# Performance work log

Hardware: AMD Instinct MI355X
Metric: run time of the kernel (lower is better)

## Reference

```python
import jax, jax.numpy as jnp
import numpy as np

B, S, EMB, H = 2, 2048, 1024, 16
D = EMB // H  # per-head dim = 64
SCALE = 1.0 / np.sqrt(D).astype(np.float32)


def setup_inputs() -> dict:
    key = jax.random.key(0)
    ks = jax.random.split(key, 11)
    lim = 1.0 / np.sqrt(EMB).astype(np.float32)  # torch Linear default init range
    def lin(kw, kb):
        W = jax.random.uniform(kw, (EMB, EMB), jnp.float32, -lim, lim)
        b = jax.random.uniform(kb, (EMB,), jnp.float32, -lim, lim)
        return W, b
    Wq, bq = lin(ks[0], ks[1])
    Wk, bk = lin(ks[2], ks[3])
    Wv, bv = lin(ks[4], ks[5])
    Wo, bo = lin(ks[6], ks[7])
    xq = jax.random.normal(ks[8], (B, S, EMB), jnp.float32)
    xk = jax.random.normal(ks[9], (B, S, EMB), jnp.float32)
    xv = jax.random.normal(ks[10], (B, S, EMB), jnp.float32)
    mask = jnp.tril(jnp.ones((S, S), dtype=jnp.int32))  # causal mask; 0 -> blocked
    return {"xq": xq, "xk": xk, "xv": xv, "mask": mask,
            "Wq": Wq, "bq": bq, "Wk": Wk, "bk": bk,
            "Wv": Wv, "bv": bv, "Wo": Wo, "bo": bo}


def reference(xq, xk, xv, mask, Wq, bq, Wk, bk, Wv, bv, Wo, bo):
    # Projections (torch Linear: x @ W.T + b), then split heads: [B,S,E] -> [B,H,S,D]
    def split_heads(x):
        return x.reshape(B, S, H, D).transpose(0, 2, 1, 3)
    Q = split_heads(xq @ Wq.T + bq)
    K = split_heads(xk @ Wk.T + bk)
    V = split_heads(xv @ Wv.T + bv)
    scores = jnp.einsum("bhqd,bhkd->bhqk", Q, K) * SCALE  # [B,H,S,S]
    scores = jnp.where(mask[None, None, :, :] == 0, jnp.float32(-1e9), scores)
    attn = jax.nn.softmax(scores, axis=-1)  # softmax over key axis (dim=2 per-head in torch)
    res = jnp.einsum("bhqk,bhkd->bhqd", attn, V)
    res = res.transpose(0, 2, 1, 3).reshape(B, S, EMB)  # merge heads back (same slicing layout)
    return res @ Wo.T + bo
```

## Files before the change

### kernel.cpp

```cpp
#include <hip/hip_runtime.h>
#include <hip/hip_bf16.h>

#define BB   2
#define SS   2048
#define EMBD 1024
#define NH   16
#define HD   64
#define QSCALE 0.18033688011112042f
#define NEG_BIG (-1e30f)

typedef __bf16 bf16;
typedef float  floatx4 __attribute__((ext_vector_type(4)));
typedef __bf16 bf16x4  __attribute__((ext_vector_type(4)));
typedef __bf16 bf16x8  __attribute__((ext_vector_type(8)));

typedef const __attribute__((address_space(1))) void* gas_ptr;
typedef __attribute__((address_space(3))) void*       las_ptr;

__device__ __forceinline__ void gl_lds16(const void* g, void* l) {
    __builtin_amdgcn_global_load_lds((gas_ptr)g, (las_ptr)l, 16, 0, 0);
}

__device__ __forceinline__ bf16x8 cvt8(const float* p) {
    bf16x8 o;
#pragma unroll
    for (int j = 0; j < 8; j++) o[j] = (bf16)p[j];
    return o;
}

__global__ __launch_bounds__(256) void cvt_all(
    const float* __restrict__ xq, const float* __restrict__ xk,
    const float* __restrict__ xv, const float* __restrict__ Wq,
    const float* __restrict__ Wk, const float* __restrict__ Wv,
    const float* __restrict__ Wo, bf16* __restrict__ xqo,
    bf16* __restrict__ xko, bf16* __restrict__ xvo, bf16* __restrict__ Wqo,
    bf16* __restrict__ Wko, bf16* __restrict__ Wvo, bf16* __restrict__ Woo) {
    const int y = blockIdx.y;
    const float* src;
    bf16* dst;
    size_t n;
    const size_t NX = (size_t)BB * SS * EMBD;
    const size_t NW = (size_t)EMBD * EMBD;
    switch (y) {
        case 0: src = xq; dst = xqo; n = NX; break;
        case 1: src = xk; dst = xko; n = NX; break;
        case 2: src = xv; dst = xvo; n = NX; break;
        case 3: src = Wq; dst = Wqo; n = NW; break;
        case 4: src = Wk; dst = Wko; n = NW; break;
        case 5: src = Wv; dst = Wvo; n = NW; break;
        default: src = Wo; dst = Woo; n = NW; break;
    }
    const size_t stride = (size_t)gridDim.x * blockDim.x * 4;
    for (size_t i = ((size_t)blockIdx.x * blockDim.x + threadIdx.x) * 4;
         i < n; i += stride) {
        floatx4 v = *(const floatx4*)(src + i);
        bf16x4 o = {(bf16)v[0], (bf16)v[1], (bf16)v[2], (bf16)v[3]};
        *(bf16x4*)(dst + i) = o;
    }
}

extern __shared__ __align__(16) char smem[];

template <int MODE, int FM>
__device__ __forceinline__ void gemm_body(const bf16* __restrict__ A,
                                          const bf16* __restrict__ W,
                                          const float* __restrict__ bias,
                                          void* __restrict__ Ov,
                                          int mBase, int nBase, float oscale) {
    constexpr int BM = 32 * FM;
    constexpr int ABYTES = BM * 64 * 2;
    bf16* As = (bf16*)smem;
    bf16* Bs = (bf16*)(smem + ABYTES);

    const int t = threadIdx.x;
    const int l = t & 63, w = t >> 6;
    const int lm = l & 15, lq = l >> 4;
    const int K = 1024;
    const int wm = (w >> 1) * (16 * FM), wn = (w & 1) * 64;

    const floatx4 zero = {0.f, 0.f, 0.f, 0.f};
    floatx4 acc[FM][4];
#pragma unroll
    for (int i = 0; i < FM; i++)
#pragma unroll
        for (int j = 0; j < 4; j++) acc[i][j] = zero;

    for (int kb = 0; kb < K; kb += 64) {
        __syncthreads();
#pragma unroll
        for (int ia = 0; ia < FM; ia++) {
            int half = ia / (FM / 2 > 0 ? FM / 2 : 1);
            int rem  = (ia % (FM / 2 > 0 ? FM / 2 : 1)) * 256 + t;
            int row  = rem >> 2;
            int col  = half * 32 + (rem & 3) * 8;
            gl_lds16(A + (size_t)(mBase + row) * K + kb + col,
                     (char*)As + (ia * 256 + w * 64) * 16);
        }
#pragma unroll
        for (int i = 0; i < 4; i++) {
            int half = i >> 1;
            int rem  = (i & 1) * 256 + t;
            int row  = rem >> 2;
            int col  = half * 32 + (rem & 3) * 8;
            gl_lds16(W + (size_t)(nBase + row) * K + kb + col,
                     (char*)Bs + (i * 256 + w * 64) * 16);
        }
        __syncthreads();

#pragma unroll
        for (int half = 0; half < 2; half++) {
            const bf16* Ah = As + half * BM * 32;
            const bf16* Bh = Bs + half * 128 * 32;
            bf16x8 af[FM], bfv[4];
#pragma unroll
            for (int f = 0; f < FM; f++)
                af[f] = *(const bf16x8*)&Ah[(wm + f * 16 + lm) * 32 + lq * 8];
#pragma unroll
            for (int f = 0; f < 4; f++)
                bfv[f] = *(const bf16x8*)&Bh[(wn + f * 16 + lm) * 32 + lq * 8];
            if (MODE == 2) {
#pragma unroll
                for (int i = 0; i < 4; i++)
#pragma unroll
                    for (int j = 0; j < FM; j++)
                        acc[j][i] = __builtin_amdgcn_mfma_f32_16x16x32_bf16(
                            bfv[i], af[j], acc[j][i], 0, 0, 0);
            } else {
#pragma unroll
                for (int fm = 0; fm < FM; fm++)
#pragma unroll
                    for (int fn = 0; fn < 4; fn++)
                        acc[fm][fn] =
                            __builtin_amdgcn_mfma_f32_16x16x32_bf16(
                                af[fm], bfv[fn], acc[fm][fn], 0, 0, 0);
            }
        }
    }

    __syncthreads();
    float* rp = (float*)smem + w * (16 * 68);

    if (MODE != 2) {
        float bvv[4];
#pragma unroll
        for (int fn = 0; fn < 4; fn++)
            bvv[fn] = bias[nBase + wn + fn * 16 + lm];
#pragma unroll
        for (int fm = 0; fm < FM; fm++) {
#pragma unroll
            for (int fn = 0; fn < 4; fn++)
#pragma unroll
                for (int r = 0; r < 4; r++)
                    rp[(lq * 4 + r) * 68 + fn * 16 + lm] =
                        (acc[fm][fn][r] + bvv[fn]) * oscale;
            if (MODE == 0) {
                int row2 = l >> 3, col8 = l & 7;
                int h = (nBase + wn) >> 6;
#pragma unroll
                for (int p = 0; p < 2; p++) {
                    int row = p * 8 + row2;
                    int m = mBase + wm + fm * 16 + row;
                    int b = m >> 11, s = m & 2047;
                    bf16x8 o = cvt8(&rp[row * 68 + col8 * 8]);
                    *(bf16x8*)((bf16*)Ov +
                               (((size_t)(b * NH + h)) * SS + s) * HD +
                               col8 * 8) = o;
                }
            } else {
                int c4 = l & 15;
#pragma unroll
                for (int p = 0; p < 4; p++) {
                    int row = p * 4 + (l >> 4);
                    int m = mBase + wm + fm * 16 + row;
                    floatx4 o = *(const floatx4*)&rp[row * 68 + c4 * 4];
                    *(floatx4*)((float*)Ov + (size_t)m * EMBD + nBase + wn +
                                c4 * 4) = o;
                }
            }
        }
    } else {
        const int b = (mBase + wm) >> 11;
        const int sbase = (mBase + wm) & 2047;
#pragma unroll
        for (int i = 0; i < 4; i++) {
            float bv[4];
#pragma unroll
            for (int r = 0; r < 4; r++)
                bv[r] = bias[nBase + wn + i * 16 + lq * 4 + r];
#pragma unroll
            for (int j = 0; j < FM; j++)
#pragma unroll
                for (int r = 0; r < 4; r++)
                    rp[(lq * 4 + r) * 68 + j * 16 + lm] =
                        acc[j][i][r] + bv[r];
            int row2 = l >> 3, col8 = l & 7;
#pragma unroll
            for (int p = 0; p < 2; p++) {
                int row = p * 8 + row2;
                int n = nBase + wn + i * 16 + row;
                int h = n >> 6, d = n & 63;
                bf16x8 o = cvt8(&rp[row * 68 + col8 * 8]);
                *(bf16x8*)((bf16*)Ov +
                           ((size_t)(b * NH + h) * HD + d) * SS + sbase +
                           col8 * 8) = o;
            }
        }
    }
}

__global__ __launch_bounds__(256, 4) void gemm_qkv(
    const bf16* __restrict__ xq, const bf16* __restrict__ xk,
    const bf16* __restrict__ xv, const bf16* __restrict__ Wq,
    const bf16* __restrict__ Wk, const bf16* __restrict__ Wv,
    const float* __restrict__ bq, const float* __restrict__ bk,
    const float* __restrict__ bv, bf16* __restrict__ Qo,
    bf16* __restrict__ Ko, bf16* __restrict__ Vo) {
    const int z = blockIdx.z;
    const int mB = blockIdx.x * 128, nB = blockIdx.y * 128;
    if (z == 0)
        gemm_body<0, 4>(xq, Wq, bq, Qo, mB, nB, QSCALE);
    else if (z == 1)
        gemm_body<0, 4>(xk, Wk, bk, Ko, mB, nB, 1.0f);
    else
        gemm_body<2, 4>(xv, Wv, bv, Vo, mB, nB, 1.0f);
}

__global__ __launch_bounds__(256, 4) void gemm_out(
    const bf16* __restrict__ A, const bf16* __restrict__ W,
    const float* __restrict__ bias, float* __restrict__ O) {
    gemm_body<1, 2>(A, W, bias, O, blockIdx.x * 64, blockIdx.y * 128, 1.0f);
}

__global__ __launch_bounds__(256, 3) void attn_fwd(
    const bf16* __restrict__ Qg, const bf16* __restrict__ Kg,
    const bf16* __restrict__ Vtg, bf16* __restrict__ Oatt) {
    __shared__ __align__(16) bf16 Ksb[2 * 64 * 64];
    __shared__ __align__(16) bf16 VTb[2 * 64 * 64];
    __shared__ __align__(16) bf16 Ps[4][16 * 64];

    const int t = threadIdx.x;
    const int l = t & 63, w = t >> 6;
    const int lm = l & 15, lq = l >> 4;
    const int m7 = lm & 7;
    const int x = blockIdx.x;
    const int i5 = x >> 5;
    const int gq = i5 >> 3, jq = i5 & 7;
    const int qt = (gq == 0) ? jq
                 : (gq == 1) ? 15 - jq
                 : (gq == 2) ? 16 + jq
                             : 31 - jq;
    const int bh = (((x >> 3) & 3) << 3) | (x & 7);
    const size_t kbase = (size_t)bh * SS * HD;
    const size_t vbase = (size_t)bh * HD * SS;
    const int b = bh >> 4, h = bh & 15;
    const floatx4 zero = {0.f, 0.f, 0.f, 0.f};

    const int trow = t >> 3, tsl = t & 7;
    const int cswz = ((tsl ^ (trow & 7)) << 3);
    const bf16* kgp = Kg + kbase + (size_t)trow * HD + cswz;
    const bf16* vgp = Vtg + vbase + (size_t)trow * SS + cswz;
    bf16* ksd = Ksb + t * 8;
    bf16* vtd = VTb + t * 8;

    bf16x8 qa0, qa1;
    {
        const bf16* qp =
            Qg + kbase + (size_t)(qt * 64 + w * 16 + lm) * HD + lq * 8;
        qa0 = *(const bf16x8*)qp;
        qa1 = *(const bf16x8*)(qp + 32);
    }

    float m_i = NEG_BIG, l_i = 0.f;
    floatx4 od[4];
#pragma unroll
    for (int dt = 0; dt < 4; dt++) od[dt] = zero;

    const int qglob = qt * 64 + w * 16 + lm;

    gl_lds16(kgp, ksd);
    gl_lds16(kgp + 2048, ksd + 2048);
    gl_lds16(vgp, vtd);
    gl_lds16(vgp + 32 * SS, vtd + 2048);
    __syncthreads();

    for (int kt = 0; kt <= qt; ++kt) {
        const int cur = kt & 1;
        const bf16* Kc = Ksb + cur * 4096;
        const bf16* Vc = VTb + cur * 4096;
        if (kt < qt) {
            const bf16* kp = kgp + (size_t)(kt + 1) * 4096;
            const bf16* vp = vgp + (size_t)(kt + 1) * 64;
            bf16* kn = ksd + (cur ^ 1) * 4096;
            bf16* vn = vtd + (cur ^ 1) * 4096;
            gl_lds16(kp, kn);
            gl_lds16(kp + 2048, kn + 2048);
            gl_lds16(vp, vn);
            gl_lds16(vp + 32 * SS, vn + 2048);
        }

        floatx4 sc[4];
#pragma unroll
        for (int j0 = 0; j0 < 4; j0++) {
            int rowK = j0 * 16 + lm;
            bf16x8 k0 = *(const bf16x8*)&Kc[rowK * 64 + ((lq ^ m7) << 3)];
            bf16x8 k1 =
                *(const bf16x8*)&Kc[rowK * 64 + (((4 + lq) ^ m7) << 3)];
            floatx4 z = zero;
            z = __builtin_amdgcn_mfma_f32_16x16x32_bf16(k0, qa0, z, 0, 0, 0);
            z = __builtin_amdgcn_mfma_f32_16x16x32_bf16(k1, qa1, z, 0, 0, 0);
            sc[j0] = z;
        }
        if (kt == qt) {
#pragma unroll
            for (int j0 = 0; j0 < 4; j0++)
#pragma unroll
                for (int r = 0; r < 4; r++) {
                    int key = kt * 64 + j0 * 16 + lq * 4 + r;
                    if (key > qglob) sc[j0][r] = NEG_BIG;
                }
        }
        float m4[4];
#pragma unroll
        for (int a = 0; a < 4; a++)
            m4[a] = fmaxf(fmaxf(sc[a][0], sc[a][1]),
                          fmaxf(sc[a][2], sc[a][3]));
        float mt = fmaxf(fmaxf(m4[0], m4[1]), fmaxf(m4[2], m4[3]));
        mt = fmaxf(mt, __shfl_xor(mt, 16));
        mt = fmaxf(mt, __shfl_xor(mt, 32));
        float mnew = fmaxf(m_i, mt);
        float alpha = __builtin_amdgcn_exp2f(m_i - mnew);
        m_i = mnew;
        float psa0 = 0.f, psa1 = 0.f, psa2 = 0.f, psa3 = 0.f;
#pragma unroll
        for (int j0 = 0; j0 < 4; j0++) {
            float p0 = __builtin_amdgcn_exp2f(sc[j0][0] - mnew);
            float p1 = __builtin_amdgcn_exp2f(sc[j0][1] - mnew);
            float p2 = __builtin_amdgcn_exp2f(sc[j0][2] - mnew);
            float p3 = __builtin_amdgcn_exp2f(sc[j0][3] - mnew);
            sc[j0][0] = p0; sc[j0][1] = p1;
            sc[j0][2] = p2; sc[j0][3] = p3;
            psa0 += p0; psa1 += p1; psa2 += p2; psa3 += p3;
        }
        float ps = (psa0 + psa1) + (psa2 + psa3);
        ps += __shfl_xor(ps, 16);
        ps += __shfl_xor(ps, 32);
        l_i = l_i * alpha + ps;
        float a0 = __shfl(alpha, lq * 4 + 0);
        float a1 = __shfl(alpha, lq * 4 + 1);
        float a2 = __shfl(alpha, lq * 4 + 2);
        float a3 = __shfl(alpha, lq * 4 + 3);
#pragma unroll
        for (int dt = 0; dt < 4; dt++) {
            od[dt][0] *= a0;
            od[dt][1] *= a1;
            od[dt][2] *= a2;
            od[dt][3] *= a3;
        }
#pragma unroll
        for (int j0l = 0; j0l < 4; j0l++) {
            floatx4 s4 = sc[j0l];
            bf16x4 pk = {(bf16)s4[0], (bf16)s4[1], (bf16)s4[2], (bf16)s4[3]};
            *(bf16x4*)&Ps[w][lm * 64 + ((j0l * 16 + lq * 4) ^ (m7 * 8))] = pk;
        }
        bf16x8 pa0 = *(const bf16x8*)&Ps[w][lm * 64 + ((lq * 8) ^ (m7 * 8))];
        bf16x8 pa1 =
            *(const bf16x8*)&Ps[w][lm * 64 + ((32 + lq * 8) ^ (m7 * 8))];
#pragma unroll
        for (int dt = 0; dt < 4; dt++) {
            int rowD = dt * 16 + lm;
            bf16x8 v0 = *(const bf16x8*)&Vc[rowD * 64 + ((lq ^ m7) << 3)];
            od[dt] = __builtin_amdgcn_mfma_f32_16x16x32_bf16(pa0, v0, od[dt],
                                                             0, 0, 0);
            bf16x8 v1 =
                *(const bf16x8*)&Vc[rowD * 64 + (((4 + lq) ^ m7) << 3)];
            od[dt] = __builtin_amdgcn_mfma_f32_16x16x32_bf16(pa1, v1, od[dt],
                                                             0, 0, 0);
        }
        __syncthreads();
    }

    float linv = 1.0f / l_i;
    float lr0 = __shfl(linv, lq * 4 + 0);
    float lr1 = __shfl(linv, lq * 4 + 1);
    float lr2 = __shfl(linv, lq * 4 + 2);
    float lr3 = __shfl(linv, lq * 4 + 3);
    float lr[4] = {lr0, lr1, lr2, lr3};
#pragma unroll
    for (int dt = 0; dt < 4; dt++) {
#pragma unroll
        for (int r = 0; r < 4; r++) {
            int s = qt * 64 + w * 16 + lq * 4 + r;
            float v = od[dt][r] * lr[r];
            Oatt[((size_t)(b * SS + s)) * EMBD + h * HD + dt * 16 + lm] =
                (bf16)v;
        }
    }
}

extern "C" void kernel_launch(void* const* d_in, const int* in_sizes, int n_in,
                              void* d_out, int out_size, void* d_ws,
                              size_t ws_size, hipStream_t stream) {
    const float* xq = (const float*)d_in[0];
    const float* xk = (const float*)d_in[1];
    const float* xv = (const float*)d_in[2];
    const float* Wq = (const float*)d_in[4];
    const float* bq = (const float*)d_in[5];
    const float* Wk = (const float*)d_in[6];
    const float* bk = (const float*)d_in[7];
    const float* Wv = (const float*)d_in[8];
    const float* bv = (const float*)d_in[9];
    const float* Wo = (const float*)d_in[10];
    const float* bo = (const float*)d_in[11];
    float* out = (float*)d_out;

    const size_t NX = (size_t)BB * SS * EMBD;
    const size_t NW = (size_t)EMBD * EMBD;
    bf16* Qw  = (bf16*)d_ws;
    bf16* Kw  = Qw + NX;
    bf16* Vw  = Kw + NX;
    bf16* Aw  = Vw + NX;
    bf16* xqb = Aw + NX;
    bf16* xkb = xqb + NX;
    bf16* xvb = xkb + NX;
    bf16* Wqb = xvb + NX;
    bf16* Wkb = Wqb + NW;
    bf16* Wvb = Wkb + NW;
    bf16* Wob = Wvb + NW;

    cvt_all<<<dim3(1024, 7), 256, 0, stream>>>(xq, xk, xv, Wq, Wk, Wv, Wo,
                                               xqb, xkb, xvb, Wqb, Wkb, Wvb,
                                               Wob);
    gemm_qkv<<<dim3(32, 8, 3), 256, 32768, stream>>>(
        xqb, xkb, xvb, Wqb, Wkb, Wvb, bq, bk, bv, Qw, Kw, Vw);
    attn_fwd<<<dim3(1024), 256, 0, stream>>>(Qw, Kw, Vw, Aw);
    gemm_out<<<dim3(64, 8), 256, 24576, stream>>>(Aw, Wob, bo, out);
}
```

Measured before the change: 224.1 us.

## Split long causal query tiles across two blocks and merge partials

The attention kernel now splits the KV range of the 16 longest query tiles into two halves run by separate blocks, writes fp32 partial outputs with row max and sum to reused workspace, and merges them in a new small kernel. This aims to balance the causal workload and shorten the critical path of the longest blocks. It also defers the online-softmax rescale unless the max grows past a threshold, and raises wave priority around MFMA sections. The cost is an extra kernel launch and fp32 partial traffic. Deferred rescaling risks exp overflow only if scores jump by a large margin.

```diff
diff --git a/kernel.cpp b/kernel.cpp
--- a/kernel.cpp
+++ b/kernel.cpp
@@ -8,6 +8,7 @@
 #define HD   64
 #define QSCALE 0.18033688011112042f
 #define NEG_BIG (-1e30f)
+#define DEFER_THR 6.0f
 
 typedef __bf16 bf16;
 typedef float  floatx4 __attribute__((ext_vector_type(4)));
@@ -233,7 +234,9 @@
 
 __global__ __launch_bounds__(256, 3) void attn_fwd(
     const bf16* __restrict__ Qg, const bf16* __restrict__ Kg,
-    const bf16* __restrict__ Vtg, bf16* __restrict__ Oatt) {
+    const bf16* __restrict__ Vtg, bf16* __restrict__ Oatt,
+    float* __restrict__ pod, float* __restrict__ pmw,
+    float* __restrict__ plw) {
     __shared__ __align__(16) bf16 Ksb[2 * 64 * 64];
     __shared__ __align__(16) bf16 VTb[2 * 64 * 64];
     __shared__ __align__(16) bf16 Ps[4][16 * 64];
@@ -244,11 +247,21 @@
     const int m7 = lm & 7;
     const int x = blockIdx.x;
     const int i5 = x >> 5;
-    const int gq = i5 >> 3, jq = i5 & 7;
-    const int qt = (gq == 0) ? jq
-                 : (gq == 1) ? 15 - jq
-                 : (gq == 2) ? 16 + jq
-                             : 31 - jq;
+    int qt, cbeg, cend, split, half;
+    if (i5 < 32) {
+        qt = 31 - (i5 >> 1);
+        half = i5 & 1;
+        int nch = qt + 1, chalf = (nch + 1) >> 1;
+        cbeg = half ? chalf : 0;
+        cend = half ? nch : chalf;
+        split = 1;
+    } else {
+        qt = 47 - i5;
+        half = 0;
+        cbeg = 0;
+        cend = qt + 1;
+        split = 0;
+    }
     const int bh = (((x >> 3) & 3) << 3) | (x & 7);
     const size_t kbase = (size_t)bh * SS * HD;
     const size_t vbase = (size_t)bh * HD * SS;
@@ -277,17 +290,17 @@
 
     const int qglob = qt * 64 + w * 16 + lm;
 
-    gl_lds16(kgp, ksd);
-    gl_lds16(kgp + 2048, ksd + 2048);
-    gl_lds16(vgp, vtd);
-    gl_lds16(vgp + 32 * SS, vtd + 2048);
+    gl_lds16(kgp + (size_t)cbeg * 4096, ksd);
+    gl_lds16(kgp + (size_t)cbeg * 4096 + 2048, ksd + 2048);
+    gl_lds16(vgp + (size_t)cbeg * 64, vtd);
+    gl_lds16(vgp + (size_t)cbeg * 64 + 32 * SS, vtd + 2048);
     __syncthreads();
 
-    for (int kt = 0; kt <= qt; ++kt) {
-        const int cur = kt & 1;
+    for (int kt = cbeg; kt < cend; ++kt) {
+        const int cur = (kt - cbeg) & 1;
         const bf16* Kc = Ksb + cur * 4096;
         const bf16* Vc = VTb + cur * 4096;
-        if (kt < qt) {
+        if (kt + 1 < cend) {
             const bf16* kp = kgp + (size_t)(kt + 1) * 4096;
             const bf16* vp = vgp + (size_t)(kt + 1) * 64;
             bf16* kn = ksd + (cur ^ 1) * 4096;
@@ -299,6 +312,7 @@
         }
 
         floatx4 sc[4];
+        __builtin_amdgcn_s_setprio(1);
 #pragma unroll
         for (int j0 = 0; j0 < 4; j0++) {
             int rowK = j0 * 16 + lm;
@@ -310,6 +324,7 @@
             z = __builtin_amdgcn_mfma_f32_16x16x32_bf16(k1, qa1, z, 0, 0, 0);
             sc[j0] = z;
         }
+        __builtin_amdgcn_s_setprio(0);
         if (kt == qt) {
 #pragma unroll
             for (int j0 = 0; j0 < 4; j0++)
@@ -327,16 +342,30 @@
         float mt = fmaxf(fmaxf(m4[0], m4[1]), fmaxf(m4[2], m4[3]));
         mt = fmaxf(mt, __shfl_xor(mt, 16));
         mt = fmaxf(mt, __shfl_xor(mt, 32));
-        float mnew = fmaxf(m_i, mt);
-        float alpha = __builtin_amdgcn_exp2f(m_i - mnew);
-        m_i = mnew;
+        if (__any(mt > m_i + DEFER_THR)) {
+            float mnew = fmaxf(m_i, mt);
+            float alpha = __builtin_amdgcn_exp2f(m_i - mnew);
+            m_i = mnew;
+            l_i *= alpha;
+            float a0 = __shfl(alpha, lq * 4 + 0);
+            float a1 = __shfl(alpha, lq * 4 + 1);
+            float a2 = __shfl(alpha, lq * 4 + 2);
+            float a3 = __shfl(alpha, lq * 4 + 3);
+#pragma unroll
+            for (int dt = 0; dt < 4; dt++) {
+                od[dt][0] *= a0;
+                od[dt][1] *= a1;
+                od[dt][2] *= a2;
+                od[dt][3] *= a3;
+            }
+        }
         float psa0 = 0.f, psa1 = 0.f, psa2 = 0.f, psa3 = 0.f;
 #pragma unroll
         for (int j0 = 0; j0 < 4; j0++) {
-            float p0 = __builtin_amdgcn_exp2f(sc[j0][0] - mnew);
-            float p1 = __builtin_amdgcn_exp2f(sc[j0][1] - mnew);
-            float p2 = __builtin_amdgcn_exp2f(sc[j0][2] - mnew);
-            float p3 = __builtin_amdgcn_exp2f(sc[j0][3] - mnew);
+            float p0 = __builtin_amdgcn_exp2f(sc[j0][0] - m_i);
+            float p1 = __builtin_amdgcn_exp2f(sc[j0][1] - m_i);
+            float p2 = __builtin_amdgcn_exp2f(sc[j0][2] - m_i);
+            float p3 = __builtin_amdgcn_exp2f(sc[j0][3] - m_i);
             sc[j0][0] = p0; sc[j0][1] = p1;
             sc[j0][2] = p2; sc[j0][3] = p3;
             psa0 += p0; psa1 += p1; psa2 += p2; psa3 += p3;
@@ -344,18 +373,7 @@
         float ps = (psa0 + psa1) + (psa2 + psa3);
         ps += __shfl_xor(ps, 16);
         ps += __shfl_xor(ps, 32);
-        l_i = l_i * alpha + ps;
-        float a0 = __shfl(alpha, lq * 4 + 0);
-        float a1 = __shfl(alpha, lq * 4 + 1);
-        float a2 = __shfl(alpha, lq * 4 + 2);
-        float a3 = __shfl(alpha, lq * 4 + 3);
-#pragma unroll
-        for (int dt = 0; dt < 4; dt++) {
-            od[dt][0] *= a0;
-            od[dt][1] *= a1;
-            od[dt][2] *= a2;
-            od[dt][3] *= a3;
-        }
+        l_i += ps;
 #pragma unroll
         for (int j0l = 0; j0l < 4; j0l++) {
             floatx4 s4 = sc[j0l];
@@ -365,6 +383,7 @@
         bf16x8 pa0 = *(const bf16x8*)&Ps[w][lm * 64 + ((lq * 8) ^ (m7 * 8))];
         bf16x8 pa1 =
             *(const bf16x8*)&Ps[w][lm * 64 + ((32 + lq * 8) ^ (m7 * 8))];
+        __builtin_amdgcn_s_setprio(1);
 #pragma unroll
         for (int dt = 0; dt < 4; dt++) {
             int rowD = dt * 16 + lm;
@@ -376,25 +395,81 @@
             od[dt] = __builtin_amdgcn_mfma_f32_16x16x32_bf16(pa1, v1, od[dt],
                                                              0, 0, 0);
         }
+        __builtin_amdgcn_s_setprio(0);
         __syncthreads();
     }
 
-    float linv = 1.0f / l_i;
-    float lr0 = __shfl(linv, lq * 4 + 0);
-    float lr1 = __shfl(linv, lq * 4 + 1);
-    float lr2 = __shfl(linv, lq * 4 + 2);
-    float lr3 = __shfl(linv, lq * 4 + 3);
-    float lr[4] = {lr0, lr1, lr2, lr3};
-#pragma unroll
-    for (int dt = 0; dt < 4; dt++) {
-#pragma unroll
-        for (int r = 0; r < 4; r++) {
-            int s = qt * 64 + w * 16 + lq * 4 + r;
-            float v = od[dt][r] * lr[r];
-            Oatt[((size_t)(b * SS + s)) * EMBD + h * HD + dt * 16 + lm] =
-                (bf16)v;
-        }
-    }
+    if (split) {
+        const int pp = (((qt - 16) << 5) | bh) * 2 + half;
+        float* po = pod + (size_t)pp * 4096;
+#pragma unroll
+        for (int dt = 0; dt < 4; dt++)
+#pragma unroll
+            for (int r = 0; r < 4; r++)
+                po[(w * 16 + lq * 4 + r) * 64 + dt * 16 + lm] = od[dt][r];
+        if (lq == 0) {
+            pmw[pp * 64 + w * 16 + lm] = m_i;
+            plw[pp * 64 + w * 16 + lm] = l_i;
+        }
+    } else {
+        float linv = 1.0f / l_i;
+        float lr0 = __shfl(linv, lq * 4 + 0);
+        float lr1 = __shfl(linv, lq * 4 + 1);
+        float lr2 = __shfl(linv, lq * 4 + 2);
+        float lr3 = __shfl(linv, lq * 4 + 3);
+        float lr[4] = {lr0, lr1, lr2, lr3};
+#pragma unroll
+        for (int dt = 0; dt < 4; dt++) {
+#pragma unroll
+            for (int r = 0; r < 4; r++) {
+                int s = qt * 64 + w * 16 + lq * 4 + r;
+                float v = od[dt][r] * lr[r];
+                Oatt[((size_t)(b * SS + s)) * EMBD + h * HD + dt * 16 + lm] =
+                    (bf16)v;
+            }
+        }
+    }
+}
+
+__global__ __launch_bounds__(256) void attn_merge(
+    const float* __restrict__ pod, const float* __restrict__ pmw,
+    const float* __restrict__ plw, bf16* __restrict__ Oatt) {
+    const int p = blockIdx.x;
+    const int qt = 16 + (p >> 5), bh = p & 31;
+    const int b = bh >> 4, h = bh & 15;
+    const int t = threadIdx.x;
+    const int q = t >> 2, d0 = (t & 3) * 16;
+    const int pp0 = p * 2, pp1 = pp0 + 1;
+    const float m0 = pmw[pp0 * 64 + q], m1 = pmw[pp1 * 64 + q];
+    const float l0 = plw[pp0 * 64 + q], l1 = plw[pp1 * 64 + q];
+    const float mm = fmaxf(m0, m1);
+    const float a0 = __builtin_amdgcn_exp2f(m0 - mm);
+    const float a1 = __builtin_amdgcn_exp2f(m1 - mm);
+    const float inv = 1.0f / (l0 * a0 + l1 * a1);
+    const float w0 = a0 * inv, w1 = a1 * inv;
+    const float* o0 = pod + ((size_t)pp0 * 64 + q) * 64 + d0;
+    const float* o1 = pod + ((size_t)pp1 * 64 + q) * 64 + d0;
+    bf16* dst =
+        Oatt + ((size_t)(b * SS + qt * 64 + q)) * EMBD + h * HD + d0;
+    bf16x8 oa, ob;
+#pragma unroll
+    for (int i = 0; i < 2; i++) {
+        floatx4 v0 = *(const floatx4*)(o0 + i * 4);
+        floatx4 v1 = *(const floatx4*)(o1 + i * 4);
+#pragma unroll
+        for (int r = 0; r < 4; r++)
+            oa[i * 4 + r] = (bf16)(v0[r] * w0 + v1[r] * w1);
+    }
+#pragma unroll
+    for (int i = 0; i < 2; i++) {
+        floatx4 v0 = *(const floatx4*)(o0 + 8 + i * 4);
+        floatx4 v1 = *(const floatx4*)(o1 + 8 + i * 4);
+#pragma unroll
+        for (int r = 0; r < 4; r++)
+            ob[i * 4 + r] = (bf16)(v0[r] * w0 + v1[r] * w1);
+    }
+    *(bf16x8*)dst = oa;
+    *(bf16x8*)(dst + 8) = ob;
 }
 
 extern "C" void kernel_launch(void* const* d_in, const int* in_sizes, int n_in,
@@ -426,12 +501,16 @@
     bf16* Wkb = Wqb + NW;
     bf16* Wvb = Wkb + NW;
     bf16* Wob = Wvb + NW;
+    float* pod = (float*)xqb;
+    float* pmw = (float*)xvb;
+    float* plw = pmw + 1024 * 64;
 
     cvt_all<<<dim3(1024, 7), 256, 0, stream>>>(xq, xk, xv, Wq, Wk, Wv, Wo,
                                                xqb, xkb, xvb, Wqb, Wkb, Wvb,
                                                Wob);
     gemm_qkv<<<dim3(32, 8, 3), 256, 32768, stream>>>(
         xqb, xkb, xvb, Wqb, Wkb, Wvb, bq, bk, bv, Qw, Kw, Vw);
-    attn_fwd<<<dim3(1024), 256, 0, stream>>>(Qw, Kw, Vw, Aw);
+    attn_fwd<<<dim3(1536), 256, 0, stream>>>(Qw, Kw, Vw, Aw, pod, pmw, plw);
+    attn_merge<<<dim3(512), 256, 0, stream>>>(pod, pmw, plw, Aw);
     gemm_out<<<dim3(64, 8), 256, 24576, stream>>>(Aw, Wob, bo, out);
 }
```

Measured after the change: 227.9 us. Within noise of the previous version (+1.7%).

## Process two query fragments per wave with 2-wave blocks and deferred rescale

Applied to the files above, without the earlier changes.

The attention kernel now runs with 128 threads (2 waves), each wave handling 32 query rows as two 16-row fragments. This reuses each K/V fragment read from LDS across two MFMAs, so LDS traffic per unit of compute drops. It also adds a lazy online-softmax rescale that skips the accumulator rescale unless the running max grows past a threshold, and uses s_setprio around the MFMA sections. In exchange each wave needs more registers and there are fewer waves per block to hide latency.

```diff
diff --git a/kernel.cpp b/kernel.cpp
--- a/kernel.cpp
+++ b/kernel.cpp
@@ -8,6 +8,7 @@
 #define HD   64
 #define QSCALE 0.18033688011112042f
 #define NEG_BIG (-1e30f)
+#define DEFER_THR 6.0f
 
 typedef __bf16 bf16;
 typedef float  floatx4 __attribute__((ext_vector_type(4)));
@@ -231,12 +232,12 @@
     gemm_body<1, 2>(A, W, bias, O, blockIdx.x * 64, blockIdx.y * 128, 1.0f);
 }
 
-__global__ __launch_bounds__(256, 3) void attn_fwd(
+__global__ __launch_bounds__(128, 2) void attn_fwd(
     const bf16* __restrict__ Qg, const bf16* __restrict__ Kg,
     const bf16* __restrict__ Vtg, bf16* __restrict__ Oatt) {
     __shared__ __align__(16) bf16 Ksb[2 * 64 * 64];
     __shared__ __align__(16) bf16 VTb[2 * 64 * 64];
-    __shared__ __align__(16) bf16 Ps[4][16 * 64];
+    __shared__ __align__(16) bf16 Ps[2][32 * 64];
 
     const int t = threadIdx.x;
     const int l = t & 63, w = t >> 6;
@@ -259,28 +260,29 @@
     const int cswz = ((tsl ^ (trow & 7)) << 3);
     const bf16* kgp = Kg + kbase + (size_t)trow * HD + cswz;
     const bf16* vgp = Vtg + vbase + (size_t)trow * SS + cswz;
-    bf16* ksd = Ksb + t * 8;
-    bf16* vtd = VTb + t * 8;
-
-    bf16x8 qa0, qa1;
-    {
-        const bf16* qp =
-            Qg + kbase + (size_t)(qt * 64 + w * 16 + lm) * HD + lq * 8;
-        qa0 = *(const bf16x8*)qp;
-        qa1 = *(const bf16x8*)(qp + 32);
-    }
-
-    float m_i = NEG_BIG, l_i = 0.f;
-    floatx4 od[4];
-#pragma unroll
-    for (int dt = 0; dt < 4; dt++) od[dt] = zero;
-
-    const int qglob = qt * 64 + w * 16 + lm;
-
-    gl_lds16(kgp, ksd);
-    gl_lds16(kgp + 2048, ksd + 2048);
-    gl_lds16(vgp, vtd);
-    gl_lds16(vgp + 32 * SS, vtd + 2048);
+
+    bf16x8 qa[2][2];
+#pragma unroll
+    for (int f = 0; f < 2; f++) {
+        const bf16* qp = Qg + kbase +
+                         (size_t)(qt * 64 + w * 32 + f * 16 + lm) * HD +
+                         lq * 8;
+        qa[f][0] = *(const bf16x8*)qp;
+        qa[f][1] = *(const bf16x8*)(qp + 32);
+    }
+
+    float m_i[2] = {NEG_BIG, NEG_BIG}, l_i[2] = {0.f, 0.f};
+    floatx4 od[2][4];
+#pragma unroll
+    for (int f = 0; f < 2; f++)
+#pragma unroll
+        for (int dt = 0; dt < 4; dt++) od[f][dt] = zero;
+
+#pragma unroll
+    for (int i = 0; i < 4; i++) {
+        gl_lds16(kgp + (size_t)i * 1024, Ksb + i * 1024 + t * 8);
+        gl_lds16(vgp + (size_t)i * 16 * SS, VTb + i * 1024 + t * 8);
+    }
     __syncthreads();
 
     for (int kt = 0; kt <= qt; ++kt) {
@@ -290,109 +292,157 @@
         if (kt < qt) {
             const bf16* kp = kgp + (size_t)(kt + 1) * 4096;
             const bf16* vp = vgp + (size_t)(kt + 1) * 64;
-            bf16* kn = ksd + (cur ^ 1) * 4096;
-            bf16* vn = vtd + (cur ^ 1) * 4096;
-            gl_lds16(kp, kn);
-            gl_lds16(kp + 2048, kn + 2048);
-            gl_lds16(vp, vn);
-            gl_lds16(vp + 32 * SS, vn + 2048);
-        }
-
-        floatx4 sc[4];
+            bf16* kn = Ksb + (cur ^ 1) * 4096 + t * 8;
+            bf16* vn = VTb + (cur ^ 1) * 4096 + t * 8;
+#pragma unroll
+            for (int i = 0; i < 4; i++) {
+                gl_lds16(kp + (size_t)i * 1024, kn + i * 1024);
+                gl_lds16(vp + (size_t)i * 16 * SS, vn + i * 1024);
+            }
+        }
+
+        floatx4 sc[2][4];
+        __builtin_amdgcn_s_setprio(1);
 #pragma unroll
         for (int j0 = 0; j0 < 4; j0++) {
             int rowK = j0 * 16 + lm;
             bf16x8 k0 = *(const bf16x8*)&Kc[rowK * 64 + ((lq ^ m7) << 3)];
             bf16x8 k1 =
                 *(const bf16x8*)&Kc[rowK * 64 + (((4 + lq) ^ m7) << 3)];
-            floatx4 z = zero;
-            z = __builtin_amdgcn_mfma_f32_16x16x32_bf16(k0, qa0, z, 0, 0, 0);
-            z = __builtin_amdgcn_mfma_f32_16x16x32_bf16(k1, qa1, z, 0, 0, 0);
-            sc[j0] = z;
-        }
+#pragma unroll
+            for (int f = 0; f < 2; f++) {
+                floatx4 z = zero;
+                z = __builtin_amdgcn_mfma_f32_16x16x32_bf16(k0, qa[f][0], z,
+                                                            0, 0, 0);
+                z = __builtin_amdgcn_mfma_f32_16x16x32_bf16(k1, qa[f][1], z,
+                                                            0, 0, 0);
+                sc[f][j0] = z;
+            }
+        }
+        __builtin_amdgcn_s_setprio(0);
         if (kt == qt) {
 #pragma unroll
-            for (int j0 = 0; j0 < 4; j0++)
-#pragma unroll
-                for (int r = 0; r < 4; r++) {
-                    int key = kt * 64 + j0 * 16 + lq * 4 + r;
-                    if (key > qglob) sc[j0][r] = NEG_BIG;
+            for (int f = 0; f < 2; f++) {
+                int qglob = qt * 64 + w * 32 + f * 16 + lm;
+#pragma unroll
+                for (int j0 = 0; j0 < 4; j0++)
+#pragma unroll
+                    for (int r = 0; r < 4; r++) {
+                        int key = kt * 64 + j0 * 16 + lq * 4 + r;
+                        if (key > qglob) sc[f][j0][r] = NEG_BIG;
+                    }
+            }
+        }
+        float mt[2];
+#pragma unroll
+        for (int f = 0; f < 2; f++) {
+            float u0 = fmaxf(fmaxf(sc[f][0][0], sc[f][0][1]),
+                             fmaxf(sc[f][0][2], sc[f][0][3]));
+            float u1 = fmaxf(fmaxf(sc[f][1][0], sc[f][1][1]),
+                             fmaxf(sc[f][1][2], sc[f][1][3]));
+            float u2 = fmaxf(fmaxf(sc[f][2][0], sc[f][2][1]),
+                             fmaxf(sc[f][2][2], sc[f][2][3]));
+            float u3 = fmaxf(fmaxf(sc[f][3][0], sc[f][3][1]),
+                             fmaxf(sc[f][3][2], sc[f][3][3]));
+            float m = fmaxf(fmaxf(u0, u1), fmaxf(u2, u3));
+            m = fmaxf(m, __shfl_xor(m, 16));
+            m = fmaxf(m, __shfl_xor(m, 32));
+            mt[f] = m;
+        }
+        bool need = (mt[0] > m_i[0] + DEFER_THR) ||
+                    (mt[1] > m_i[1] + DEFER_THR);
+        if (__any(need)) {
+#pragma unroll
+            for (int f = 0; f < 2; f++) {
+                float mnew = fmaxf(m_i[f], mt[f]);
+                float alpha = __builtin_amdgcn_exp2f(m_i[f] - mnew);
+                m_i[f] = mnew;
+                l_i[f] *= alpha;
+                float a0 = __shfl(alpha, lq * 4 + 0);
+                float a1 = __shfl(alpha, lq * 4 + 1);
+                float a2 = __shfl(alpha, lq * 4 + 2);
+                float a3 = __shfl(alpha, lq * 4 + 3);
+#pragma unroll
+                for (int dt = 0; dt < 4; dt++) {
+                    od[f][dt][0] *= a0;
+                    od[f][dt][1] *= a1;
+                    od[f][dt][2] *= a2;
+                    od[f][dt][3] *= a3;
                 }
-        }
-        float m4[4];
-#pragma unroll
-        for (int a = 0; a < 4; a++)
-            m4[a] = fmaxf(fmaxf(sc[a][0], sc[a][1]),
-                          fmaxf(sc[a][2], sc[a][3]));
-        float mt = fmaxf(fmaxf(m4[0], m4[1]), fmaxf(m4[2], m4[3]));
-        mt = fmaxf(mt, __shfl_xor(mt, 16));
-        mt = fmaxf(mt, __shfl_xor(mt, 32));
-        float mnew = fmaxf(m_i, mt);
-        float alpha = __builtin_amdgcn_exp2f(m_i - mnew);
-        m_i = mnew;
-        float psa0 = 0.f, psa1 = 0.f, psa2 = 0.f, psa3 = 0.f;
-#pragma unroll
-        for (int j0 = 0; j0 < 4; j0++) {
-            float p0 = __builtin_amdgcn_exp2f(sc[j0][0] - mnew);
-            float p1 = __builtin_amdgcn_exp2f(sc[j0][1] - mnew);
-            float p2 = __builtin_amdgcn_exp2f(sc[j0][2] - mnew);
-            float p3 = __builtin_amdgcn_exp2f(sc[j0][3] - mnew);
-            sc[j0][0] = p0; sc[j0][1] = p1;
-            sc[j0][2] = p2; sc[j0][3] = p3;
-            psa0 += p0; psa1 += p1; psa2 += p2; psa3 += p3;
-        }
-        float ps = (psa0 + psa1) + (psa2 + psa3);
-        ps += __shfl_xor(ps, 16);
-        ps += __shfl_xor(ps, 32);
-        l_i = l_i * alpha + ps;
-        float a0 = __shfl(alpha, lq * 4 + 0);
-        float a1 = __shfl(alpha, lq * 4 + 1);
-        float a2 = __shfl(alpha, lq * 4 + 2);
-        float a3 = __shfl(alpha, lq * 4 + 3);
-#pragma unroll
-        for (int dt = 0; dt < 4; dt++) {
-            od[dt][0] *= a0;
-            od[dt][1] *= a1;
-            od[dt][2] *= a2;
-            od[dt][3] *= a3;
-        }
-#pragma unroll
-        for (int j0l = 0; j0l < 4; j0l++) {
-            floatx4 s4 = sc[j0l];
-            bf16x4 pk = {(bf16)s4[0], (bf16)s4[1], (bf16)s4[2], (bf16)s4[3]};
-            *(bf16x4*)&Ps[w][lm * 64 + ((j0l * 16 + lq * 4) ^ (m7 * 8))] = pk;
-        }
-        bf16x8 pa0 = *(const bf16x8*)&Ps[w][lm * 64 + ((lq * 8) ^ (m7 * 8))];
-        bf16x8 pa1 =
-            *(const bf16x8*)&Ps[w][lm * 64 + ((32 + lq * 8) ^ (m7 * 8))];
+            }
+        }
+#pragma unroll
+        for (int f = 0; f < 2; f++) {
+            float psa0 = 0.f, psa1 = 0.f, psa2 = 0.f, psa3 = 0.f;
+#pragma unroll
+            for (int j0 = 0; j0 < 4; j0++) {
+                float p0 = __builtin_amdgcn_exp2f(sc[f][j0][0] - m_i[f]);
+                float p1 = __builtin_amdgcn_exp2f(sc[f][j0][1] - m_i[f]);
+                float p2 = __builtin_amdgcn_exp2f(sc[f][j0][2] - m_i[f]);
+                float p3 = __builtin_amdgcn_exp2f(sc[f][j0][3] - m_i[f]);
+                sc[f][j0][0] = p0; sc[f][j0][1] = p1;
+                sc[f][j0][2] = p2; sc[f][j0][3] = p3;
+                psa0 += p0; psa1 += p1; psa2 += p2; psa3 += p3;
+            }
+            float ps = (psa0 + psa1) + (psa2 + psa3);
+            ps += __shfl_xor(ps, 16);
+            ps += __shfl_xor(ps, 32);
+            l_i[f] += ps;
+        }
+#pragma unroll
+        for (int f = 0; f < 2; f++)
+#pragma unroll
+            for (int j0 = 0; j0 < 4; j0++) {
+                floatx4 s4 = sc[f][j0];
+                bf16x4 pk = {(bf16)s4[0], (bf16)s4[1], (bf16)s4[2],
+                             (bf16)s4[3]};
+                *(bf16x4*)&Ps[w][(f * 16 + lm) * 64 +
+                                 ((j0 * 16 + lq * 4) ^ (m7 * 8))] = pk;
+            }
+        bf16x8 pa[2][2];
+#pragma unroll
+        for (int f = 0; f < 2; f++) {
+            pa[f][0] = *(const bf16x8*)&Ps[w][(f * 16 + lm) * 64 +
+                                              ((lq * 8) ^ (m7 * 8))];
+            pa[f][1] = *(const bf16x8*)&Ps[w][(f * 16 + lm) * 64 +
+                                              ((32 + lq * 8) ^ (m7 * 8))];
+        }
+        __builtin_amdgcn_s_setprio(1);
 #pragma unroll
         for (int dt = 0; dt < 4; dt++) {
             int rowD = dt * 16 + lm;
             bf16x8 v0 = *(const bf16x8*)&Vc[rowD * 64 + ((lq ^ m7) << 3)];
-            od[dt] = __builtin_amdgcn_mfma_f32_16x16x32_bf16(pa0, v0, od[dt],
-                                                             0, 0, 0);
             bf16x8 v1 =
                 *(const bf16x8*)&Vc[rowD * 64 + (((4 + lq) ^ m7) << 3)];
-            od[dt] = __builtin_amdgcn_mfma_f32_16x16x32_bf16(pa1, v1, od[dt],
-                                                             0, 0, 0);
-        }
+#pragma unroll
+            for (int f = 0; f < 2; f++) {
+                od[f][dt] = __builtin_amdgcn_mfma_f32_16x16x32_bf16(
+                    pa[f][0], v0, od[f][dt], 0, 0, 0);
+                od[f][dt] = __builtin_amdgcn_mfma_f32_16x16x32_bf16(
+                    pa[f][1], v1, od[f][dt], 0, 0, 0);
+            }
+        }
+        __builtin_amdgcn_s_setprio(0);
         __syncthreads();
     }
 
-    float linv = 1.0f / l_i;
-    float lr0 = __shfl(linv, lq * 4 + 0);
-    float lr1 = __shfl(linv, lq * 4 + 1);
-    float lr2 = __shfl(linv, lq * 4 + 2);
-    float lr3 = __shfl(linv, lq * 4 + 3);
-    float lr[4] = {lr0, lr1, lr2, lr3};
-#pragma unroll
-    for (int dt = 0; dt < 4; dt++) {
-#pragma unroll
-        for (int r = 0; r < 4; r++) {
-            int s = qt * 64 + w * 16 + lq * 4 + r;
-            float v = od[dt][r] * lr[r];
-            Oatt[((size_t)(b * SS + s)) * EMBD + h * HD + dt * 16 + lm] =
-                (bf16)v;
+#pragma unroll
+    for (int f = 0; f < 2; f++) {
+        float linv = 1.0f / l_i[f];
+        float lr0 = __shfl(linv, lq * 4 + 0);
+        float lr1 = __shfl(linv, lq * 4 + 1);
+        float lr2 = __shfl(linv, lq * 4 + 2);
+        float lr3 = __shfl(linv, lq * 4 + 3);
+        float lr[4] = {lr0, lr1, lr2, lr3};
+#pragma unroll
+        for (int dt = 0; dt < 4; dt++) {
+#pragma unroll
+            for (int r = 0; r < 4; r++) {
+                int s = qt * 64 + w * 32 + f * 16 + lq * 4 + r;
+                float v = od[f][dt][r] * lr[r];
+                Oatt[((size_t)(b * SS + s)) * EMBD + h * HD + dt * 16 + lm] =
+                    (bf16)v;
+            }
         }
     }
 }
@@ -432,6 +482,6 @@
                                                Wob);
     gemm_qkv<<<dim3(32, 8, 3), 256, 32768, stream>>>(
         xqb, xkb, xvb, Wqb, Wkb, Wvb, bq, bk, bv, Qw, Kw, Vw);
-    attn_fwd<<<dim3(1024), 256, 0, stream>>>(Qw, Kw, Vw, Aw);
+    attn_fwd<<<dim3(1024), 128, 0, stream>>>(Qw, Kw, Vw, Aw);
     gemm_out<<<dim3(64, 8), 256, 24576, stream>>>(Aw, Wob, bo, out);
 }
```

Result: no change. 225.4 us (+0.6%).
